# Optimization experiments

Hardware: AMD Instinct MI355X
Metric: run time of the kernel (lower is better)

The kernel has to match this reference:

```python
import jax, jax.numpy as jnp
import numpy as np

B, T, DM, H, D = 4, 2048, 1024, 16, 64
INNER = H * D


def setup_inputs() -> dict:
    key = jax.random.key(0)
    ks = jax.random.split(key, 8)
    s = 0.02
    x = jax.random.normal(ks[0], (B, T, DM), dtype=jnp.float32)
    state = jnp.zeros((B, H, D, D), dtype=jnp.float32)
    Wq = jax.random.normal(ks[1], (DM, INNER), dtype=jnp.float32) * s
    Wk = jax.random.normal(ks[2], (DM, INNER), dtype=jnp.float32) * s
    Wv = jax.random.normal(ks[3], (DM, INNER), dtype=jnp.float32) * s
    Wa = jax.random.normal(ks[4], (DM, H), dtype=jnp.float32) * s
    ba = jnp.zeros((H,), dtype=jnp.float32)
    Wb = jax.random.normal(ks[5], (DM, H), dtype=jnp.float32) * s
    bb = jnp.zeros((H,), dtype=jnp.float32)  # beta_init=0.5 -> logit(0.5)=0
    Wo = jax.random.normal(ks[6], (INNER, DM), dtype=jnp.float32) * s
    return {"x": x, "state": state, "Wq": Wq, "Wk": Wk, "Wv": Wv,
            "Wa": Wa, "ba": ba, "Wb": Wb, "bb": bb, "Wo": Wo}


def reference(x, state, Wq, Wk, Wv, Wa, ba, Wb, bb, Wo):
    Bb, Tt, _ = x.shape
    Q = (x @ Wq).reshape(Bb, Tt, H, D)
    K = (x @ Wk).reshape(Bb, Tt, H, D)
    V = (x @ Wv).reshape(Bb, Tt, H, D)
    alpha = jax.nn.sigmoid(x @ Wa + ba)  # (B,T,H) forget gate
    beta = jax.nn.sigmoid(x @ Wb + bb)   # (B,T,H) write gate
    # F.normalize(p=2, dim=-1) with eps=1e-12 clamp on the norm
    K = K / jnp.maximum(jnp.linalg.norm(K, axis=-1, keepdims=True), 1e-12)

    def step(S, inp):
        qt, kt, vt, at, bt = inp  # (B,H,D),(B,H,D),(B,H,D),(B,H),(B,H)
        S = at[..., None, None] * S + bt[..., None, None] * jnp.einsum('bhi,bhj->bhij', vt, kt)
        yt = jnp.einsum('bhij,bhj->bhi', S, qt)
        return S, yt

    xs = (jnp.swapaxes(Q, 0, 1), jnp.swapaxes(K, 0, 1), jnp.swapaxes(V, 0, 1),
          jnp.swapaxes(alpha, 0, 1), jnp.swapaxes(beta, 0, 1))
    S, ys = jax.lax.scan(step, state, xs)  # ys: (T,B,H,D)
    out = jnp.swapaxes(ys, 0, 1).reshape(Bb, Tt, INNER) @ Wo
    return out, S
```

## Files before the change

### kernel.cpp

```cpp
#include <hip/hip_runtime.h>
#include <hip/hip_bf16.h>
#include <math.h>

#define B_SZ   4
#define T_LEN  2048
#define DM     1024
#define NH     16
#define DH     64
#define INNER  1024
#define NROWS  (B_SZ*T_LEN)
#define NQ     (NROWS*INNER)
#define CH     64
#define NCH    (T_LEN/CH)

typedef __bf16 bf16x8 __attribute__((ext_vector_type(8)));
typedef __bf16 bf16x4 __attribute__((ext_vector_type(4)));
typedef float  f32x4  __attribute__((ext_vector_type(4)));
typedef __attribute__((address_space(3))) void*       lds_vp;
typedef const __attribute__((address_space(1))) void* gbl_vp;

__device__ __forceinline__ int swz(int row, int col) {
    return (row << 6) + ((((col >> 3) + (row >> 2)) & 7) << 3) + (col & 7);
}

__global__ __launch_bounds__(256) void wt_cast_transpose(const float* __restrict__ Wq,
                                                         const float* __restrict__ Wk,
                                                         const float* __restrict__ Wv,
                                                         const float* __restrict__ Wo,
                                                         __bf16* __restrict__ WqT,
                                                         __bf16* __restrict__ WkT,
                                                         __bf16* __restrict__ WvT,
                                                         __bf16* __restrict__ WoT) {
    __shared__ float tile[64][65];
    const float* W;
    __bf16* WT;
    if      (blockIdx.z == 0) { W = Wq; WT = WqT; }
    else if (blockIdx.z == 1) { W = Wk; WT = WkT; }
    else if (blockIdx.z == 2) { W = Wv; WT = WvT; }
    else                      { W = Wo; WT = WoT; }

    const int k0 = blockIdx.y * 64, n0 = blockIdx.x * 64;
    const int tr  = threadIdx.x >> 4;
    const int tc4 = (threadIdx.x & 15) * 4;

#pragma unroll
    for (int r = 0; r < 4; r++) {
        const int k = tr + 16 * r;
        const float4 v = *(const float4*)(W + (size_t)(k0 + k) * DM + n0 + tc4);
        tile[k][tc4 + 0] = v.x;
        tile[k][tc4 + 1] = v.y;
        tile[k][tc4 + 2] = v.z;
        tile[k][tc4 + 3] = v.w;
    }
    __syncthreads();
#pragma unroll
    for (int r = 0; r < 4; r++) {
        const int n = tr + 16 * r;
        bf16x4 o;
#pragma unroll
        for (int j = 0; j < 4; j++) o[j] = (__bf16)tile[tc4 + j][n];
        *(bf16x4*)(WT + (size_t)(n0 + n) * DM + k0 + tc4) = o;
    }
}

#define AOF(b_, kh_) ((b_) * 32768 + (kh_) * 16384)
#define BOF(b_, kh_) (98304 + (b_) * 16384 + (kh_) * 8192)

template <typename CT>
__device__ __forceinline__ void gemm_8ph_body(const __bf16* __restrict__ A,
                                              const __bf16* __restrict__ BT,
                                              CT* __restrict__ C,
                                              int m0, int n0bt, int n0c) {
    __shared__ __align__(16) char lds[147456];

    const int tid  = threadIdx.x;
    const int wid  = tid >> 6;
    const int lane = tid & 63;
    const int wm = wid >> 1;
    const int wn = wid & 1;
    const int frow = lane & 15, quad = lane >> 4;

    int offA[4], offB[4];
#pragma unroll
    for (int i = 0; i < 4; ++i) {
        const int ra = wm * 64 + i * 16 + frow;
        offA[i] = ra * 64 + ((quad ^ ((ra >> 1) & 3)) << 4);
        const int rb = wn * 64 + i * 16 + frow;
        offB[i] = rb * 64 + ((quad ^ ((rb >> 1) & 3)) << 4);
    }

    const int lr = lane >> 2;
    const int cs = ((lane & 3) ^ ((lane >> 3) & 3)) << 3;
    const __bf16* gA0 = A  + (size_t)(m0 + (wid * 2 + 0) * 16 + lr) * 1024 + cs;
    const __bf16* gA1 = A  + (size_t)(m0 + (wid * 2 + 1) * 16 + lr) * 1024 + cs;
    const __bf16* gB  = BT + (size_t)(n0bt + wid * 16 + lr) * 1024 + cs;

#define STG3(t_, kh_, b_) do {                                                     \
        __builtin_amdgcn_global_load_lds((gbl_vp)(gA0 + (size_t)(t_) * 64 + (kh_) * 32), \
            (lds_vp)(lds + AOF(b_, kh_) + (wid * 2 + 0) * 1024), 16, 0, 0);        \
        __builtin_amdgcn_global_load_lds((gbl_vp)(gA1 + (size_t)(t_) * 64 + (kh_) * 32), \
            (lds_vp)(lds + AOF(b_, kh_) + (wid * 2 + 1) * 1024), 16, 0, 0);        \
        __builtin_amdgcn_global_load_lds((gbl_vp)(gB  + (size_t)(t_) * 64 + (kh_) * 32), \
            (lds_vp)(lds + BOF(b_, kh_) + wid * 1024), 16, 0, 0);                  \
    } while (0)

#define VM9 asm volatile("s_waitcnt vmcnt(9)" ::: "memory")
#define VM6 asm volatile("s_waitcnt vmcnt(6)" ::: "memory")
#define VM3 asm volatile("s_waitcnt vmcnt(3)" ::: "memory")
#define VM0 asm volatile("s_waitcnt vmcnt(0)" ::: "memory")

    f32x4 acc[4][4];
#pragma unroll
    for (int i = 0; i < 4; i++)
#pragma unroll
        for (int j = 0; j < 4; j++) acc[i][j] = (f32x4)0.f;

    STG3(0, 0, 0); STG3(0, 1, 0); STG3(1, 0, 1); STG3(1, 1, 1);
    VM9;
    asm volatile("s_barrier" ::: "memory");

#define PH(b_, kh_, STG_STMT, VM_STMT)                                             \
    {                                                                              \
        const char* Ab_ = lds + AOF(b_, kh_);                                      \
        const char* Bb_ = lds + BOF(b_, kh_);                                      \
        bf16x8 af_[4], bfr_[4];                                                    \
        _Pragma("unroll")                                                          \
        for (int i_ = 0; i_ < 4; ++i_) {                                           \
            af_[i_]  = *(const bf16x8*)(Ab_ + offA[i_]);                           \
            bfr_[i_] = *(const bf16x8*)(Bb_ + offB[i_]);                           \
        }                                                                          \
        STG_STMT;                                                                  \
        asm volatile("s_barrier" ::: "memory");                                    \
        asm volatile("s_waitcnt lgkmcnt(0)" ::: "memory");                         \
        __builtin_amdgcn_sched_barrier(0);                                         \
        __builtin_amdgcn_s_setprio(1);                                             \
        _Pragma("unroll")                                                          \
        for (int mi_ = 0; mi_ < 4; ++mi_)                                          \
            _Pragma("unroll")                                                      \
            for (int nj_ = 0; nj_ < 4; ++nj_)                                      \
                acc[mi_][nj_] = __builtin_amdgcn_mfma_f32_16x16x32_bf16(           \
                    af_[mi_], bfr_[nj_], acc[mi_][nj_], 0, 0, 0);                  \
        __builtin_amdgcn_s_setprio(0);                                             \
        VM_STMT;                                                                   \
        asm volatile("s_barrier" ::: "memory");                                    \
    }

    for (int u = 0; u < 12; u += 3) {
        PH(0, 0, STG3(u + 2, 0, 2), VM9);  PH(0, 1, STG3(u + 2, 1, 2), VM9);
        PH(1, 0, STG3(u + 3, 0, 0), VM9);  PH(1, 1, STG3(u + 3, 1, 0), VM9);
        PH(2, 0, STG3(u + 4, 0, 1), VM9);  PH(2, 1, STG3(u + 4, 1, 1), VM9);
    }
    PH(0, 0, STG3(14, 0, 2), VM9);  PH(0, 1, STG3(14, 1, 2), VM9);
    PH(1, 0, STG3(15, 0, 0), VM9);  PH(1, 1, STG3(15, 1, 0), VM9);
    PH(2, 0, , VM6);                PH(2, 1, , VM3);
    PH(0, 0, , VM0);                PH(0, 1, , );

#undef PH
#undef STG3
#undef VM9
#undef VM6
#undef VM3
#undef VM0

    const int cr = quad * 4, cc = frow;
#pragma unroll
    for (int mi = 0; mi < 4; ++mi) {
#pragma unroll
        for (int nj = 0; nj < 4; ++nj) {
            CT* Cp = C + (size_t)(m0 + wm * 64 + mi * 16 + cr) * 1024
                       + n0c + wn * 64 + nj * 16 + cc;
#pragma unroll
            for (int r = 0; r < 4; r++) Cp[(size_t)r * 1024] = (CT)acc[mi][nj][r];
        }
    }
}

__global__ __launch_bounds__(512, 2) void qkv_gemm_8ph(const __bf16* __restrict__ xb,
                                                       const __bf16* __restrict__ BTall,
                                                       __bf16* __restrict__ QKV) {
    const int id = blockIdx.x;
    const int wg = (id & 7) * 96 + (id >> 3);
    const int mt = wg / 24, nt = wg % 24;
    const int mat = nt >> 3;
    gemm_8ph_body<__bf16>(xb, BTall, QKV + (size_t)mat * NQ,
                          mt * 256, nt * 128, (nt & 7) * 128);
}

__global__ __launch_bounds__(512, 2) void out_gemm_8ph(const __bf16* __restrict__ Yb,
                                                       const __bf16* __restrict__ WoT,
                                                       float* __restrict__ Cout) {
    const int id = blockIdx.x;
    const int wg = (id & 7) * 32 + (id >> 3);
    const int mt = wg >> 3, nt = wg & 7;
    gemm_8ph_body<float>(Yb, WoT, Cout, mt * 256, nt * 128, nt * 128);
}

#define WGS 1032
#define LAS 40
__global__ __launch_bounds__(256) void gates_fused(const float* __restrict__ x,
                                                   const float* __restrict__ Wa,
                                                   const float* __restrict__ ba,
                                                   const float* __restrict__ Wb,
                                                   const float* __restrict__ bb,
                                                   float* __restrict__ AlphaT,
                                                   float* __restrict__ BetaT,
                                                   __bf16* __restrict__ xb) {
    __shared__ __align__(16) __bf16 lWg[32 * WGS];
    __shared__ __align__(16) __bf16 lA[64 * LAS];

    const int tid = threadIdx.x;
    const int wid = tid >> 6, lane = tid & 63;
    const int quad = lane >> 4, frow = lane & 15;
    const int m0 = blockIdx.x * 64;

    {
        const int kbase = tid * 4;
#pragma unroll
        for (int j = 0; j < 4; j++) {
            const int k = kbase + j;
            const float4* war = (const float4*)(Wa + (size_t)k * NH);
            const float4* wbr = (const float4*)(Wb + (size_t)k * NH);
#pragma unroll
            for (int q = 0; q < 4; q++) {
                const float4 a = war[q], bq = wbr[q];
                lWg[(q * 4 + 0) * WGS + k] = (__bf16)a.x;
                lWg[(q * 4 + 1) * WGS + k] = (__bf16)a.y;
                lWg[(q * 4 + 2) * WGS + k] = (__bf16)a.z;
                lWg[(q * 4 + 3) * WGS + k] = (__bf16)a.w;
                lWg[(16 + q * 4 + 0) * WGS + k] = (__bf16)bq.x;
                lWg[(16 + q * 4 + 1) * WGS + k] = (__bf16)bq.y;
                lWg[(16 + q * 4 + 2) * WGS + k] = (__bf16)bq.z;
                lWg[(16 + q * 4 + 3) * WGS + k] = (__bf16)bq.w;
            }
        }
    }
    const float bias_a = ba[frow];
    const float bias_b = bb[frow];

    const int rrow = tid >> 2;
    const int rk   = (tid & 3) * 8;
    const float* xrow = x + (size_t)(m0 + rrow) * DM + rk;
    float4 c0 = *(const float4*)(xrow + 0);
    float4 c1 = *(const float4*)(xrow + 4);

    f32x4 acc[2];
    acc[0] = (f32x4)0.f; acc[1] = (f32x4)0.f;

    for (int k0 = 0; k0 < DM; k0 += 32) {
        __syncthreads();
        bf16x8 xv;
        xv[0] = (__bf16)c0.x; xv[1] = (__bf16)c0.y; xv[2] = (__bf16)c0.z; xv[3] = (__bf16)c0.w;
        xv[4] = (__bf16)c1.x; xv[5] = (__bf16)c1.y; xv[6] = (__bf16)c1.z; xv[7] = (__bf16)c1.w;
        *(bf16x8*)&lA[rrow * LAS + rk] = xv;
        *(bf16x8*)(xb + (size_t)(m0 + rrow) * DM + k0 + rk) = xv;
        if (k0 + 32 < DM) {
            c0 = *(const float4*)(xrow + k0 + 32);
            c1 = *(const float4*)(xrow + k0 + 36);
        }
        __syncthreads();
        const bf16x8 af = *(const bf16x8*)&lA[(wid * 16 + frow) * LAS + quad * 8];
#pragma unroll
        for (int ct = 0; ct < 2; ct++) {
            const bf16x8 bf = *(const bf16x8*)&lWg[(ct * 16 + frow) * WGS + k0 + quad * 8];
            acc[ct] = __builtin_amdgcn_mfma_f32_16x16x32_bf16(af, bf, acc[ct], 0, 0, 0);
        }
    }

#pragma unroll
    for (int ct = 0; ct < 2; ct++) {
        const float bias = (ct == 0) ? bias_a : bias_b;
        float* dst = (ct == 0) ? AlphaT : BetaT;
#pragma unroll
        for (int r = 0; r < 4; r++) {
            const int row = m0 + wid * 16 + quad * 4 + r;
            const float s = acc[ct][r] + bias;
            dst[(size_t)frow * NROWS + row] = 1.f / (1.f + __expf(-s));
        }
    }
}

__global__ __launch_bounds__(256) void chunk_ds(const __bf16* __restrict__ Q,
                                                const __bf16* __restrict__ K,
                                                __bf16* __restrict__ V,
                                                const float* __restrict__ AlphaT,
                                                const float* __restrict__ BetaT,
                                                float* __restrict__ Dec,
                                                float* __restrict__ DS,
                                                float* __restrict__ ExpT) {
    __shared__ __align__(16) __bf16 Qb[64 * 64];
    __shared__ __align__(16) __bf16 Kb[64 * 64];
    __shared__ __align__(16) __bf16 KTs[64 * 64];
    __shared__ __align__(16) __bf16 VTb[64 * 64];
    __shared__ __align__(16) __bf16 Ab[64 * 64];
    __shared__ float sla[64], sb[64], swd[64];

    const int blk = blockIdx.x;
    const int c = blk & 31, h = (blk >> 5) & 15, b = blk >> 9;
    const int t0 = c * CH;
    const int tid = threadIdx.x;
    const int wid = tid >> 6, lane = tid & 63;
    const size_t rowbase = ((size_t)(b * T_LEN + t0) * NH + h) * DH;

    const int srow = tid >> 3;
    const int scol = (tid & 7) * 8;
    bf16x8 q8[2], k8[2], v8[2];
#pragma unroll
    for (int r = 0; r < 2; r++) {
        const size_t g = rowbase + (size_t)(srow + 32 * r) * INNER + scol;
        q8[r] = *(const bf16x8*)(Q + g);
        k8[r] = *(const bf16x8*)(K + g);
        v8[r] = *(const bf16x8*)(V + g);
    }

    if (tid < 64) {
        const int t = tid;
        const size_t gaT = (size_t)h * NROWS + b * T_LEN + t0 + t;
        const float a  = AlphaT[gaT];
        const float bt = BetaT[gaT];
        float xx = logf(a);
#pragma unroll
        for (int off = 1; off < 64; off <<= 1) {
            const float y = __shfl_up(xx, off, 64);
            if (t >= off) xx += y;
        }
        const float la63 = __shfl(xx, 63, 64);
        sla[t] = xx;
        sb[t]  = bt;
        swd[t] = bt * __expf(la63 - xx);
        ExpT[gaT] = __expf(xx);
        if (t == 63) Dec[(size_t)(b * NH + h) * NCH + c] = __expf(la63);
    }
    __syncthreads();

#pragma unroll
    for (int r = 0; r < 2; r++) {
        const int row = srow + 32 * r;
        float kf[8];
        float ss = 0.f;
#pragma unroll
        for (int j = 0; j < 8; j++) { kf[j] = (float)k8[r][j]; ss += kf[j] * kf[j]; }
        ss += __shfl_xor(ss, 1, 64);
        ss += __shfl_xor(ss, 2, 64);
        ss += __shfl_xor(ss, 4, 64);
        const float scale = 1.f / fmaxf(sqrtf(ss), 1e-12f);
        const float w = swd[row];
        bf16x8 kn8;
#pragma unroll
        for (int j = 0; j < 8; j++) {
            const float kn = kf[j] * scale;
            kn8[j] = (__bf16)kn;
            KTs[swz(scol + j, row)] = (__bf16)(w * kn);
            VTb[swz(scol + j, row)] = v8[r][j];
        }
        *(bf16x8*)&Qb[swz(row, scol)] = q8[r];
        *(bf16x8*)&Kb[swz(row, scol)] = kn8;
    }
    __syncthreads();

    const int quad = lane >> 4;
    const int frow = lane & 15;
    const int tw = wid * 16;

    f32x4 accG[4];
#pragma unroll
    for (int i = 0; i < 4; i++) accG[i] = (f32x4)0.f;
#pragma unroll
    for (int ks = 0; ks < 2; ks++) {
        const int ko = quad * 8 + 32 * ks;
        const bf16x8 aq = *(const bf16x8*)&Qb[swz(tw + frow, ko)];
#pragma unroll
        for (int st = 0; st < 4; st++) {
            const bf16x8 bk = *(const bf16x8*)&Kb[swz(st * 16 + frow, ko)];
            accG[st] = __builtin_amdgcn_mfma_f32_16x16x32_bf16(aq, bk, accG[st], 0, 0, 0);
        }
    }
#pragma unroll
    for (int st = 0; st < 4; st++) {
#pragma unroll
        for (int r = 0; r < 4; r++) {
            const int t = tw + quad * 4 + r;
            const int s = st * 16 + frow;
            const float av = (s <= t) ? __expf(sla[t] - sla[s]) * sb[s] * accG[st][r] : 0.f;
            Ab[swz(t, s)] = (__bf16)av;
        }
    }
    __syncthreads();

    f32x4 accY[4], accD[4];
#pragma unroll
    for (int i = 0; i < 4; i++) { accY[i] = (f32x4)0.f; accD[i] = (f32x4)0.f; }
#pragma unroll
    for (int ks = 0; ks < 2; ks++) {
        const int ko = quad * 8 + 32 * ks;
        const bf16x8 aA = *(const bf16x8*)&Ab[swz(tw + frow, ko)];
        const bf16x8 aV = *(const bf16x8*)&VTb[swz(tw + frow, ko)];
#pragma unroll
        for (int jt = 0; jt < 4; jt++) {
            const bf16x8 bv = *(const bf16x8*)&VTb[swz(jt * 16 + frow, ko)];
            const bf16x8 bk = *(const bf16x8*)&KTs[swz(jt * 16 + frow, ko)];
            accY[jt] = __builtin_amdgcn_mfma_f32_16x16x32_bf16(aA, bv, accY[jt], 0, 0, 0);
            accD[jt] = __builtin_amdgcn_mfma_f32_16x16x32_bf16(aV, bk, accD[jt], 0, 0, 0);
        }
    }
#pragma unroll
    for (int jt = 0; jt < 4; jt++) {
#pragma unroll
        for (int r = 0; r < 4; r++) {
            const int row = tw + quad * 4 + r;
            const size_t g = rowbase + (size_t)row * INNER + jt * 16 + frow;
            V[g]  = (__bf16)accY[jt][r];
            DS[g] = accD[jt][r];
        }
    }
}

__global__ __launch_bounds__(256) void chunk_state(const float* __restrict__ DS,
                                                   const float* __restrict__ Dec,
                                                   const float* __restrict__ state_in,
                                                   float* __restrict__ state_out,
                                                   __bf16* __restrict__ ScB) {
    const int blk = blockIdx.x;
    const int b = blk >> 4, h = blk & 15;
    const int tid = threadIdx.x;
    const int w = tid >> 6;
    const int l = tid & 63;

    float S[16];
    {
        const float* st = state_in + ((size_t)(b * NH + h) * DH + l) * DH + 16 * w;
#pragma unroll
        for (int j4 = 0; j4 < 4; j4++)
            *(float4*)&S[4 * j4] = *(const float4*)(st + 4 * j4);
    }

    for (int c = 0; c < NCH; c++) {
        const int t0 = c * CH;
        const float decay = Dec[(size_t)(b * NH + h) * NCH + c];
        const size_t off = ((size_t)(b * T_LEN + t0 + l) * NH + h) * DH + 16 * w;
        const float* ds = DS + off;
        __bf16* sc = ScB + off;
        float4 dv[4];
#pragma unroll
        for (int j4 = 0; j4 < 4; j4++) dv[j4] = *(const float4*)(ds + 4 * j4);
#pragma unroll
        for (int j4 = 0; j4 < 4; j4++) {
            bf16x4 o;
            o[0] = (__bf16)S[4 * j4 + 0]; o[1] = (__bf16)S[4 * j4 + 1];
            o[2] = (__bf16)S[4 * j4 + 2]; o[3] = (__bf16)S[4 * j4 + 3];
            *(bf16x4*)(sc + 4 * j4) = o;
        }
#pragma unroll
        for (int j4 = 0; j4 < 4; j4++) {
            S[4 * j4 + 0] = decay * S[4 * j4 + 0] + dv[j4].x;
            S[4 * j4 + 1] = decay * S[4 * j4 + 1] + dv[j4].y;
            S[4 * j4 + 2] = decay * S[4 * j4 + 2] + dv[j4].z;
            S[4 * j4 + 3] = decay * S[4 * j4 + 3] + dv[j4].w;
        }
    }

    float* so = state_out + ((size_t)(b * NH + h) * DH + l) * DH + 16 * w;
#pragma unroll
    for (int j4 = 0; j4 < 4; j4++)
        *(float4*)(so + 4 * j4) = *(const float4*)&S[4 * j4];
}

__global__ __launch_bounds__(256) void chunk_y(const __bf16* __restrict__ Q,
                                               const __bf16* __restrict__ ScB,
                                               __bf16* __restrict__ Yb,
                                               const float* __restrict__ ExpT) {
    __shared__ __align__(16) __bf16 Qb[64 * 64];
    __shared__ __align__(16) __bf16 Scb[64 * 64];
    __shared__ float sexp[64];

    const int blk = blockIdx.x;
    const int c = blk & 31, h = (blk >> 5) & 15, b = blk >> 9;
    const int t0 = c * CH;
    const int tid = threadIdx.x;
    const int wid = tid >> 6, lane = tid & 63;
    const size_t rowbase = ((size_t)(b * T_LEN + t0) * NH + h) * DH;

    const int srow = tid >> 3;
    const int scol = (tid & 7) * 8;
    bf16x8 q8[2], s8[2];
#pragma unroll
    for (int r = 0; r < 2; r++) {
        const size_t g = rowbase + (size_t)(srow + 32 * r) * INNER + scol;
        q8[r] = *(const bf16x8*)(Q + g);
        s8[r] = *(const bf16x8*)(ScB + g);
    }

    if (tid < 64)
        sexp[tid] = ExpT[(size_t)h * NROWS + b * T_LEN + t0 + tid];

#pragma unroll
    for (int r = 0; r < 2; r++) {
        *(bf16x8*)&Qb[swz(srow + 32 * r, scol)]  = q8[r];
        *(bf16x8*)&Scb[swz(srow + 32 * r, scol)] = s8[r];
    }
    __syncthreads();

    const int quad = lane >> 4;
    const int frow = lane & 15;
    const int tw = wid * 16;

    f32x4 accU[4];
#pragma unroll
    for (int i = 0; i < 4; i++) accU[i] = (f32x4)0.f;
#pragma unroll
    for (int ks = 0; ks < 2; ks++) {
        const int ko = quad * 8 + 32 * ks;
        const bf16x8 aq = *(const bf16x8*)&Qb[swz(tw + frow, ko)];
#pragma unroll
        for (int it = 0; it < 4; it++) {
            const bf16x8 bs = *(const bf16x8*)&Scb[swz(it * 16 + frow, ko)];
            accU[it] = __builtin_amdgcn_mfma_f32_16x16x32_bf16(aq, bs, accU[it], 0, 0, 0);
        }
    }

#pragma unroll
    for (int it = 0; it < 4; it++) {
#pragma unroll
        for (int r = 0; r < 4; r++) {
            const int t = tw + quad * 4 + r;
            const size_t g = rowbase + (size_t)t * INNER + it * 16 + frow;
            Yb[g] = (__bf16)(sexp[t] * accU[it][r] + (float)Yb[g]);
        }
    }
}

extern "C" void kernel_launch(void* const* d_in, const int* in_sizes, int n_in,
                              void* d_out, int out_size, void* d_ws, size_t ws_size,
                              hipStream_t stream) {
    const float* x     = (const float*)d_in[0];
    const float* state = (const float*)d_in[1];
    const float* Wq    = (const float*)d_in[2];
    const float* Wk    = (const float*)d_in[3];
    const float* Wv    = (const float*)d_in[4];
    const float* Wa    = (const float*)d_in[5];
    const float* ba    = (const float*)d_in[6];
    const float* Wb    = (const float*)d_in[7];
    const float* bb    = (const float*)d_in[8];
    const float* Wo    = (const float*)d_in[9];

    __bf16* Qb    = (__bf16*)d_ws;
    __bf16* Kbf   = Qb + (size_t)NQ;
    __bf16* Vbf   = Kbf + (size_t)NQ;
    float*  DS    = (float*)(Vbf + (size_t)NQ);
    float*  AlphaT= DS + (size_t)NQ;
    float*  BetaT = AlphaT + (size_t)NROWS * NH;
    float*  ExpT  = BetaT + (size_t)NROWS * NH;
    float*  Dec   = ExpT + (size_t)NROWS * NH;
    __bf16* xb    = (__bf16*)(Dec + (size_t)B_SZ * NH * NCH);
    __bf16* ScB   = xb;
    __bf16* WqT   = xb + (size_t)NQ;
    __bf16* WkT   = WqT + (size_t)DM * INNER;
    __bf16* WvT   = WkT + (size_t)DM * INNER;
    __bf16* WoT   = WvT + (size_t)DM * INNER;

    float* out  = (float*)d_out;
    float* Sout = out + (size_t)NQ;

    wt_cast_transpose<<<dim3(16, 16, 4), 256, 0, stream>>>(Wq, Wk, Wv, Wo,
                                                           WqT, WkT, WvT, WoT);
    gates_fused<<<NROWS / 64, 256, 0, stream>>>(x, Wa, ba, Wb, bb,
                                                AlphaT, BetaT, xb);
    qkv_gemm_8ph<<<768, 512, 0, stream>>>(xb, WqT, Qb);
    chunk_ds<<<B_SZ * NH * NCH, 256, 0, stream>>>(Qb, Kbf, Vbf, AlphaT, BetaT,
                                                  Dec, DS, ExpT);
    chunk_state<<<B_SZ * NH, 256, 0, stream>>>(DS, Dec, state, Sout, ScB);
    chunk_y<<<B_SZ * NH * NCH, 256, 0, stream>>>(Qb, ScB, Vbf, ExpT);
    out_gemm_8ph<<<256, 512, 0, stream>>>(Vbf, WoT, out);
}
```

Baseline: 287.0 us.

## Rework GEMM pipeline to 4 waves with 128x64 per-wave tiles and single K-32 stages

```diff
diff --git a/kernel.cpp b/kernel.cpp
--- a/kernel.cpp
+++ b/kernel.cpp
@@ -63,15 +63,15 @@
     }
 }
 
-#define AOF(b_, kh_) ((b_) * 32768 + (kh_) * 16384)
-#define BOF(b_, kh_) (98304 + (b_) * 16384 + (kh_) * 8192)
+#define STAGE_STRIDE 24576
+#define B_BASE 16384
 
 template <typename CT>
-__device__ __forceinline__ void gemm_8ph_body(const __bf16* __restrict__ A,
-                                              const __bf16* __restrict__ BT,
-                                              CT* __restrict__ C,
-                                              int m0, int n0bt, int n0c) {
-    __shared__ __align__(16) char lds[147456];
+__device__ __forceinline__ void gemm_pipe_body(const __bf16* __restrict__ A,
+                                               const __bf16* __restrict__ BT,
+                                               CT* __restrict__ C,
+                                               int m0, int n0bt, int n0c) {
+    __shared__ __align__(16) char lds[3 * STAGE_STRIDE];
 
     const int tid  = threadIdx.x;
     const int wid  = tid >> 6;
@@ -80,62 +80,70 @@
     const int wn = wid & 1;
     const int frow = lane & 15, quad = lane >> 4;
 
-    int offA[4], offB[4];
-#pragma unroll
-    for (int i = 0; i < 4; ++i) {
-        const int ra = wm * 64 + i * 16 + frow;
+    int offA[8], offB[4];
+#pragma unroll
+    for (int i = 0; i < 8; ++i) {
+        const int ra = wm * 128 + i * 16 + frow;
         offA[i] = ra * 64 + ((quad ^ ((ra >> 1) & 3)) << 4);
-        const int rb = wn * 64 + i * 16 + frow;
-        offB[i] = rb * 64 + ((quad ^ ((rb >> 1) & 3)) << 4);
+    }
+#pragma unroll
+    for (int j = 0; j < 4; ++j) {
+        const int rb = wn * 64 + j * 16 + frow;
+        offB[j] = B_BASE + rb * 64 + ((quad ^ ((rb >> 1) & 3)) << 4);
     }
 
     const int lr = lane >> 2;
     const int cs = ((lane & 3) ^ ((lane >> 3) & 3)) << 3;
-    const __bf16* gA0 = A  + (size_t)(m0 + (wid * 2 + 0) * 16 + lr) * 1024 + cs;
-    const __bf16* gA1 = A  + (size_t)(m0 + (wid * 2 + 1) * 16 + lr) * 1024 + cs;
-    const __bf16* gB  = BT + (size_t)(n0bt + wid * 16 + lr) * 1024 + cs;
-
-#define STG3(t_, kh_, b_) do {                                                     \
-        __builtin_amdgcn_global_load_lds((gbl_vp)(gA0 + (size_t)(t_) * 64 + (kh_) * 32), \
-            (lds_vp)(lds + AOF(b_, kh_) + (wid * 2 + 0) * 1024), 16, 0, 0);        \
-        __builtin_amdgcn_global_load_lds((gbl_vp)(gA1 + (size_t)(t_) * 64 + (kh_) * 32), \
-            (lds_vp)(lds + AOF(b_, kh_) + (wid * 2 + 1) * 1024), 16, 0, 0);        \
-        __builtin_amdgcn_global_load_lds((gbl_vp)(gB  + (size_t)(t_) * 64 + (kh_) * 32), \
-            (lds_vp)(lds + BOF(b_, kh_) + wid * 1024), 16, 0, 0);                  \
+    const __bf16* gA[4];
+#pragma unroll
+    for (int q = 0; q < 4; ++q)
+        gA[q] = A + (size_t)(m0 + wid * 64 + q * 16 + lr) * 1024 + cs;
+    const __bf16* gB[2];
+#pragma unroll
+    for (int q = 0; q < 2; ++q)
+        gB[q] = BT + (size_t)(n0bt + wid * 32 + q * 16 + lr) * 1024 + cs;
+
+#define STG(t_, b_) do {                                                           \
+        _Pragma("unroll")                                                          \
+        for (int q_ = 0; q_ < 4; ++q_)                                             \
+            __builtin_amdgcn_global_load_lds((gbl_vp)(gA[q_] + (size_t)(t_) * 32), \
+                (lds_vp)(lds + (b_) * STAGE_STRIDE + (wid * 64 + q_ * 16) * 64),   \
+                16, 0, 0);                                                         \
+        _Pragma("unroll")                                                          \
+        for (int q_ = 0; q_ < 2; ++q_)                                             \
+            __builtin_amdgcn_global_load_lds((gbl_vp)(gB[q_] + (size_t)(t_) * 32), \
+                (lds_vp)(lds + (b_) * STAGE_STRIDE + B_BASE + (wid * 32 + q_ * 16) * 64), \
+                16, 0, 0);                                                         \
     } while (0)
 
-#define VM9 asm volatile("s_waitcnt vmcnt(9)" ::: "memory")
 #define VM6 asm volatile("s_waitcnt vmcnt(6)" ::: "memory")
-#define VM3 asm volatile("s_waitcnt vmcnt(3)" ::: "memory")
 #define VM0 asm volatile("s_waitcnt vmcnt(0)" ::: "memory")
 
-    f32x4 acc[4][4];
-#pragma unroll
-    for (int i = 0; i < 4; i++)
+    f32x4 acc[8][4];
+#pragma unroll
+    for (int i = 0; i < 8; i++)
 #pragma unroll
         for (int j = 0; j < 4; j++) acc[i][j] = (f32x4)0.f;
 
-    STG3(0, 0, 0); STG3(0, 1, 0); STG3(1, 0, 1); STG3(1, 1, 1);
-    VM9;
+    STG(0, 0); STG(1, 1);
+    VM6;
     asm volatile("s_barrier" ::: "memory");
 
-#define PH(b_, kh_, STG_STMT, VM_STMT)                                             \
+#define PH(b_, STG_STMT, VM_STMT)                                                  \
     {                                                                              \
-        const char* Ab_ = lds + AOF(b_, kh_);                                      \
-        const char* Bb_ = lds + BOF(b_, kh_);                                      \
-        bf16x8 af_[4], bfr_[4];                                                    \
+        const char* Sb_ = lds + (b_) * STAGE_STRIDE;                               \
+        bf16x8 af_[8], bfr_[4];                                                    \
         _Pragma("unroll")                                                          \
-        for (int i_ = 0; i_ < 4; ++i_) {                                           \
-            af_[i_]  = *(const bf16x8*)(Ab_ + offA[i_]);                           \
-            bfr_[i_] = *(const bf16x8*)(Bb_ + offB[i_]);                           \
-        }                                                                          \
+        for (int i_ = 0; i_ < 8; ++i_) af_[i_]  = *(const bf16x8*)(Sb_ + offA[i_]);\
+        _Pragma("unroll")                                                          \
+        for (int j_ = 0; j_ < 4; ++j_) bfr_[j_] = *(const bf16x8*)(Sb_ + offB[j_]);\
         STG_STMT;                                                                  \
         asm volatile("s_barrier" ::: "memory");                                    \
         asm volatile("s_waitcnt lgkmcnt(0)" ::: "memory");                         \
         __builtin_amdgcn_sched_barrier(0);                                         \
         __builtin_amdgcn_s_setprio(1);                                             \
         _Pragma("unroll")                                                          \
-        for (int mi_ = 0; mi_ < 4; ++mi_)                                          \
+        for (int mi_ = 0; mi_ < 8; ++mi_)                                          \
             _Pragma("unroll")                                                      \
             for (int nj_ = 0; nj_ < 4; ++nj_)                                      \
                 acc[mi_][nj_] = __builtin_amdgcn_mfma_f32_16x16x32_bf16(           \
@@ -145,29 +153,26 @@
         asm volatile("s_barrier" ::: "memory");                                    \
     }
 
-    for (int u = 0; u < 12; u += 3) {
-        PH(0, 0, STG3(u + 2, 0, 2), VM9);  PH(0, 1, STG3(u + 2, 1, 2), VM9);
-        PH(1, 0, STG3(u + 3, 0, 0), VM9);  PH(1, 1, STG3(u + 3, 1, 0), VM9);
-        PH(2, 0, STG3(u + 4, 0, 1), VM9);  PH(2, 1, STG3(u + 4, 1, 1), VM9);
-    }
-    PH(0, 0, STG3(14, 0, 2), VM9);  PH(0, 1, STG3(14, 1, 2), VM9);
-    PH(1, 0, STG3(15, 0, 0), VM9);  PH(1, 1, STG3(15, 1, 0), VM9);
-    PH(2, 0, , VM6);                PH(2, 1, , VM3);
-    PH(0, 0, , VM0);                PH(0, 1, , );
+    for (int u = 0; u < 10; ++u) {
+        const int p = 3 * u;
+        PH(0, STG(p + 2, 2), VM6);
+        PH(1, STG(p + 3, 0), VM6);
+        PH(2, STG(p + 4, 1), VM6);
+    }
+    PH(0, , VM0);
+    PH(1, , );
 
 #undef PH
-#undef STG3
-#undef VM9
+#undef STG
 #undef VM6
-#undef VM3
 #undef VM0
 
     const int cr = quad * 4, cc = frow;
 #pragma unroll
-    for (int mi = 0; mi < 4; ++mi) {
+    for (int mi = 0; mi < 8; ++mi) {
 #pragma unroll
         for (int nj = 0; nj < 4; ++nj) {
-            CT* Cp = C + (size_t)(m0 + wm * 64 + mi * 16 + cr) * 1024
+            CT* Cp = C + (size_t)(m0 + wm * 128 + mi * 16 + cr) * 1024
                        + n0c + wn * 64 + nj * 16 + cc;
 #pragma unroll
             for (int r = 0; r < 4; r++) Cp[(size_t)r * 1024] = (CT)acc[mi][nj][r];
@@ -175,24 +180,24 @@
     }
 }
 
-__global__ __launch_bounds__(512, 2) void qkv_gemm_8ph(const __bf16* __restrict__ xb,
+__global__ __launch_bounds__(256, 2) void qkv_gemm_8ph(const __bf16* __restrict__ xb,
                                                        const __bf16* __restrict__ BTall,
                                                        __bf16* __restrict__ QKV) {
     const int id = blockIdx.x;
     const int wg = (id & 7) * 96 + (id >> 3);
     const int mt = wg / 24, nt = wg % 24;
     const int mat = nt >> 3;
-    gemm_8ph_body<__bf16>(xb, BTall, QKV + (size_t)mat * NQ,
-                          mt * 256, nt * 128, (nt & 7) * 128);
-}
-
-__global__ __launch_bounds__(512, 2) void out_gemm_8ph(const __bf16* __restrict__ Yb,
+    gemm_pipe_body<__bf16>(xb, BTall, QKV + (size_t)mat * NQ,
+                           mt * 256, nt * 128, (nt & 7) * 128);
+}
+
+__global__ __launch_bounds__(256, 2) void out_gemm_8ph(const __bf16* __restrict__ Yb,
                                                        const __bf16* __restrict__ WoT,
                                                        float* __restrict__ Cout) {
     const int id = blockIdx.x;
     const int wg = (id & 7) * 32 + (id >> 3);
     const int mt = wg >> 3, nt = wg & 7;
-    gemm_8ph_body<float>(Yb, WoT, Cout, mt * 256, nt * 128, nt * 128);
+    gemm_pipe_body<float>(Yb, WoT, Cout, mt * 256, nt * 128, nt * 128);
 }
 
 #define WGS 1032
@@ -564,10 +569,10 @@
                                                            WqT, WkT, WvT, WoT);
     gates_fused<<<NROWS / 64, 256, 0, stream>>>(x, Wa, ba, Wb, bb,
                                                 AlphaT, BetaT, xb);
-    qkv_gemm_8ph<<<768, 512, 0, stream>>>(xb, WqT, Qb);
+    qkv_gemm_8ph<<<768, 256, 0, stream>>>(xb, WqT, Qb);
     chunk_ds<<<B_SZ * NH * NCH, 256, 0, stream>>>(Qb, Kbf, Vbf, AlphaT, BetaT,
                                                   Dec, DS, ExpT);
     chunk_state<<<B_SZ * NH, 256, 0, stream>>>(DS, Dec, state, Sout, ScB);
     chunk_y<<<B_SZ * NH * NCH, 256, 0, stream>>>(Qb, ScB, Vbf, ExpT);
-    out_gemm_8ph<<<256, 512, 0, stream>>>(Vbf, WoT, out);
-}
+    out_gemm_8ph<<<256, 256, 0, stream>>>(Vbf, WoT, out);
+}
```

After: 278.6 us. 2.9% less time.
